# Kernel tuning notes

Measured on AMD Instinct MI355X. Metric: run time of the kernel, lower is better.

The kernel has to match this reference:

```python
import jax, jax.numpy as jnp
import numpy as np

N = 500_000
IN_CH = 64
OUT_CH = 32
HEADS = 4
NUM_SEGS = 1024


def setup_inputs() -> dict:
    key = jax.random.key(0)
    ks = jax.random.split(key, 8)
    x = jax.random.normal(ks[0], (N, IN_CH), dtype=jnp.float32)
    batch = jnp.sort(jax.random.randint(ks[1], (N,), 0, NUM_SEGS, dtype=jnp.int32))
    batch = batch.at[-1].set(NUM_SEGS - 1)  # mimic size = batch[-1]+1 == NUM_SEGS
    s_in = 1.0 / np.sqrt(IN_CH)
    s_hg = 1.0 / np.sqrt(HEADS * IN_CH)
    s_hm = 1.0 / np.sqrt(OUT_CH * HEADS)
    # gate_nn: Linear(in, heads*in, bias=False) -> PReLU -> Linear(heads*in, heads, bias=False)
    gate_w1 = jax.random.uniform(ks[2], (HEADS * IN_CH, IN_CH), jnp.float32, -s_in, s_in)
    prelu_a = jnp.asarray(0.25, dtype=jnp.float32)
    gate_w2 = jax.random.uniform(ks[3], (HEADS, HEADS * IN_CH), jnp.float32, -s_hg, s_hg)
    # nn: Linear(in, out*heads) -> ReLU -> Linear(out*heads, out*heads)
    mlp_w1 = jax.random.uniform(ks[4], (OUT_CH * HEADS, IN_CH), jnp.float32, -s_in, s_in)
    mlp_b1 = jax.random.uniform(ks[5], (OUT_CH * HEADS,), jnp.float32, -s_in, s_in)
    mlp_w2 = jax.random.uniform(ks[6], (OUT_CH * HEADS, OUT_CH * HEADS), jnp.float32, -s_hm, s_hm)
    mlp_b2 = jax.random.uniform(ks[7], (OUT_CH * HEADS,), jnp.float32, -s_hm, s_hm)
    return {"x": x, "batch": batch, "num_segments": NUM_SEGS,
            "gate_w1": gate_w1, "prelu_a": prelu_a, "gate_w2": gate_w2,
            "mlp_w1": mlp_w1, "mlp_b1": mlp_b1, "mlp_w2": mlp_w2, "mlp_b2": mlp_b2}


def reference(x, batch, num_segments, gate_w1, prelu_a, gate_w2,
              mlp_w1, mlp_b1, mlp_w2, mlp_b2):
    n = x.shape[0]
    # gate network: [N, heads]
    h = x @ gate_w1.T
    h = jnp.where(h >= 0, h, prelu_a * h)  # PReLU (shared scalar slope)
    gate = h @ gate_w2.T
    # feature MLP: [N, heads, out]
    feat = jax.nn.relu(x @ mlp_w1.T + mlp_b1) @ mlp_w2.T + mlp_b2
    feat = feat.reshape(n, HEADS, -1)
    # segment (per-graph) softmax over nodes, per head
    gmax = jax.ops.segment_max(gate, batch, num_segments=num_segments)  # [S, heads]
    escore = jnp.exp(gate - gmax[batch])
    denom = jax.ops.segment_sum(escore, batch, num_segments=num_segments)
    score = escore / (denom[batch] + 1e-16)  # [N, heads]
    # weighted scatter-add pooling
    out = jax.ops.segment_sum(score[..., None] * feat, batch, num_segments=num_segments)
    return out.reshape(num_segments, -1)  # [S, heads*out]
```

## Files before the change

kernel.cpp:

```cpp
#include <hip/hip_runtime.h>
#include <cstdint>
#include <cstddef>

#define NN 500000
#define NG 15625
#define NBLK 1536
#define NWAVES (NBLK * 2)

typedef __attribute__((ext_vector_type(8))) short short8;
typedef __attribute__((ext_vector_type(4))) float floatx4;
typedef __attribute__((ext_vector_type(4))) float fv4;

__device__ __forceinline__ unsigned short f2bf(float f) {
  union { float f; unsigned u; } v; v.f = f;
  unsigned r = v.u + 0x7FFFu + ((v.u >> 16) & 1u);
  return (unsigned short)(r >> 16);
}
__device__ __forceinline__ unsigned cvtpk(float a, float b) {
  unsigned r;
  asm("v_cvt_pk_bf16_f32 %0, %1, %2" : "=v"(r) : "v"(a), "v"(b));
  return r;
}
__device__ __forceinline__ fv4 ntload4(const float* p) {
  return __builtin_nontemporal_load((const fv4*)p);
}
__device__ __forceinline__ float bflo(unsigned u) {
  union { unsigned u; float f; } v; v.u = u << 16; return v.f;
}
__device__ __forceinline__ float bfhi(unsigned u) {
  union { unsigned u; float f; } v; v.u = u & 0xffff0000u; return v.f;
}

#define MFMA16(a, b, c) __builtin_amdgcn_mfma_f32_16x16x32_bf16((a), (b), (c), 0, 0, 0)

__global__ void swizzle_weights(const float* __restrict__ gw1, const float* __restrict__ mw1,
                                const float* __restrict__ gw2,
                                unsigned short* __restrict__ gw1s,
                                unsigned short* __restrict__ mw1s,
                                unsigned short* __restrict__ gw2s,
                                float* __restrict__ denom, float* __restrict__ zws) {
  int e = blockIdx.x * 256 + threadIdx.x;
  if (e < 4096) denom[e] = 0.f;
#pragma unroll
  for (int i = 0; i < 19; ++i) {
    int o = e + i * 28672;
    if (o < 524288) zws[o] = 0.f;
  }
  if (e >= 24576) {
    int local = e - 24576;
    int j = local & 7, lane = (local >> 3) & 63, s = local >> 9;
    int row = lane & 15, quad = (lane >> 4) & 3;
    int w = s * 32 + ((j >> 2) << 4) + 4 * quad + (j & 3);
    gw2s[local] = (row < 4) ? f2bf(gw2[row * 256 + w]) : (unsigned short)0;
    return;
  }
  const float* src; unsigned short* dst; int local;
  if (e < 16384) { src = gw1; dst = gw1s; local = e; }
  else           { src = mw1; dst = mw1s; local = e - 16384; }
  int j = local & 7, lane = (local >> 3) & 63, tile = local >> 9;
  int ks = tile & 1, mtile = tile >> 1;
  int row = mtile * 16 + (lane & 15);
  int k   = ks * 32 + ((lane >> 4) & 3) * 8 + j;
  dst[local] = f2bf(src[row * 64 + k]);
}

#define FLUSH() do {                                                          \
  if (quad == 0) {                                                            \
    _Pragma("unroll") for (int mt_ = 0; mt_ < 8; ++mt_)                       \
      _Pragma("unroll") for (int r_ = 0; r_ < 4; ++r_)                        \
        atomicAdd(&zws[((size_t)cur_seg * 4 + r_) * 128 + mt_ * 16 + lcol],   \
                  acc[mt_][r_]);                                              \
  }                                                                           \
  _Pragma("unroll") for (int mt_ = 0; mt_ < 8; ++mt_)                         \
    acc[mt_] = (floatx4){0.f, 0.f, 0.f, 0.f};                                 \
  { float v_ = es; v_ += __shfl_xor(v_, 16); v_ += __shfl_xor(v_, 32);        \
    if (lane < 4) atomicAdd(&denom[cur_seg * 4 + lane], v_); }                \
  es = 0.f;                                                                   \
} while (0)

__global__ __launch_bounds__(128, 2) void fused_kernel(
    const float* __restrict__ x, const int* __restrict__ batch,
    const unsigned short* __restrict__ gw1s, const unsigned short* __restrict__ mw1s,
    const unsigned short* __restrict__ gw2s, const float* __restrict__ prelu_a,
    const float* __restrict__ b1, float* __restrict__ denom,
    float* __restrict__ zws) {
  const int t = threadIdx.x;
  const int wave = t >> 6, lane = t & 63;
  const int quad = lane >> 4, lcol = lane & 15;

  const float slope = prelu_a[0];
  const int W = blockIdx.x * 2 + wave;
  const int g0 = (int)(((long long)W * NG) / NWAVES);
  const int g1 = (int)(((long long)(W + 1) * NG) / NWAVES);

  float b1v[8];
#pragma unroll
  for (int mt = 0; mt < 8; ++mt) b1v[mt] = b1[mt * 16 + lcol];

  floatx4 acc[8];
#pragma unroll
  for (int mt = 0; mt < 8; ++mt) acc[mt] = (floatx4){0.f, 0.f, 0.f, 0.f};
  float es = 0.f;
  int fs = g0 * 32; if (fs > NN - 1) fs = NN - 1;
  int cur_seg = batch[fs];

  for (int g = g0; g < g1; ++g) {
    const int base = g * 32;
    int sv[2];
    short8 bx[2][2];
#pragma unroll
    for (int nt = 0; nt < 2; ++nt) {
      int node = base + nt * 16 + lcol;
      sv[nt] = batch[node];
      const float* xp = x + (size_t)node * 64 + quad * 8;
      fv4 v0 = ntload4(xp), v1 = ntload4(xp + 4);
      fv4 v2 = ntload4(xp + 32), v3 = ntload4(xp + 36);
      union { short8 s; unsigned u[4]; } u0, u1;
      u0.u[0] = cvtpk(v0[0], v0[1]); u0.u[1] = cvtpk(v0[2], v0[3]);
      u0.u[2] = cvtpk(v1[0], v1[1]); u0.u[3] = cvtpk(v1[2], v1[3]);
      u1.u[0] = cvtpk(v2[0], v2[1]); u1.u[1] = cvtpk(v2[2], v2[3]);
      u1.u[2] = cvtpk(v3[0], v3[1]); u1.u[3] = cvtpk(v3[2], v3[3]);
      bx[nt][0] = u0.s; bx[nt][1] = u1.s;
    }

    floatx4 cg0 = {0.f, 0.f, 0.f, 0.f}, cg1 = {0.f, 0.f, 0.f, 0.f};
#pragma unroll
    for (int sst = 0; sst < 8; ++sst) {
      union GB { short8 s; unsigned u[4]; } gb0, gb1;
#pragma unroll
      for (int half = 0; half < 2; ++half) {
        const int mt = sst * 2 + half;
        short8 a0 = *(const short8*)(gw1s + ((size_t)(mt * 2 + 0) * 64 + lane) * 8);
        short8 a1 = *(const short8*)(gw1s + ((size_t)(mt * 2 + 1) * 64 + lane) * 8);
        floatx4 c0 = {0.f, 0.f, 0.f, 0.f};
        c0 = MFMA16(a0, bx[0][0], c0);
        c0 = MFMA16(a1, bx[0][1], c0);
        floatx4 c1 = {0.f, 0.f, 0.f, 0.f};
        c1 = MFMA16(a0, bx[1][0], c1);
        c1 = MFMA16(a1, bx[1][1], c1);
        gb0.u[half * 2 + 0] = cvtpk(fmaxf(c0[0], slope * c0[0]),
                                    fmaxf(c0[1], slope * c0[1]));
        gb0.u[half * 2 + 1] = cvtpk(fmaxf(c0[2], slope * c0[2]),
                                    fmaxf(c0[3], slope * c0[3]));
        gb1.u[half * 2 + 0] = cvtpk(fmaxf(c1[0], slope * c1[0]),
                                    fmaxf(c1[1], slope * c1[1]));
        gb1.u[half * 2 + 1] = cvtpk(fmaxf(c1[2], slope * c1[2]),
                                    fmaxf(c1[3], slope * c1[3]));
      }
      short8 ga = *(const short8*)(gw2s + ((size_t)sst * 64 + lane) * 8);
      cg0 = MFMA16(ga, gb0.s, cg0);
      cg1 = MFMA16(ga, gb1.s, cg1);
    }
    float e0a[4], e1a[4];
#pragma unroll
    for (int hh = 0; hh < 4; ++hh) {
      e0a[hh] = __expf(cg0[hh]);
      e1a[hh] = __expf(cg1[hh]);
    }

    float ev[8]; int svb[8];
#pragma unroll
    for (int j = 0; j < 4; ++j) {
      int src = 4 * quad + j;
      svb[j]     = __shfl(sv[0], src);
      svb[4 + j] = __shfl(sv[1], src);
      float t0 = __shfl(e0a[0], src), t1 = __shfl(e0a[1], src);
      float t2 = __shfl(e0a[2], src), t3 = __shfl(e0a[3], src);
      float c01 = (lcol & 1) ? t1 : t0, c23 = (lcol & 1) ? t3 : t2;
      ev[j] = (lcol & 2) ? c23 : c01;
      t0 = __shfl(e1a[0], src); t1 = __shfl(e1a[1], src);
      t2 = __shfl(e1a[2], src); t3 = __shfl(e1a[3], src);
      c01 = (lcol & 1) ? t1 : t0; c23 = (lcol & 1) ? t3 : t2;
      ev[4 + j] = (lcol & 2) ? c23 : c01;
    }

    union BH { short8 s; unsigned u[4]; } zb[8];
#pragma unroll
    for (int mt = 0; mt < 8; ++mt) {
      short8 w0 = *(const short8*)(mw1s + ((size_t)(mt * 2 + 0) * 64 + lane) * 8);
      short8 w1 = *(const short8*)(mw1s + ((size_t)(mt * 2 + 1) * 64 + lane) * 8);
      float bb = b1v[mt];
      floatx4 c0 = {0.f, 0.f, 0.f, 0.f};
      c0 = MFMA16(bx[0][0], w0, c0);
      c0 = MFMA16(bx[0][1], w1, c0);
      floatx4 c1 = {0.f, 0.f, 0.f, 0.f};
      c1 = MFMA16(bx[1][0], w0, c1);
      c1 = MFMA16(bx[1][1], w1, c1);
      zb[mt].u[0] = cvtpk(fmaxf(c0[0] + bb, 0.f), fmaxf(c0[1] + bb, 0.f));
      zb[mt].u[1] = cvtpk(fmaxf(c0[2] + bb, 0.f), fmaxf(c0[3] + bb, 0.f));
      zb[mt].u[2] = cvtpk(fmaxf(c1[0] + bb, 0.f), fmaxf(c1[1] + bb, 0.f));
      zb[mt].u[3] = cvtpk(fmaxf(c1[2] + bb, 0.f), fmaxf(c1[3] + bb, 0.f));
    }

    int p = 0;
    while (p < 32) {
      int selv = (p >> 4) ? sv[1] : sv[0];
      int s = __shfl(selv, p & 15);
      if (s != cur_seg) { FLUSH(); cur_seg = s; }
      int cnt = (int)__popcll(__ballot(sv[0] == s)) +
                (int)__popcll(__ballot(sv[1] == s));
      union { unsigned u[4]; short8 s8; } ea;
#pragma unroll
      for (int jj = 0; jj < 4; ++jj) {
        float e0 = (lcol < 4 && svb[2 * jj] == s) ? ev[2 * jj] : 0.f;
        float e1 = (lcol < 4 && svb[2 * jj + 1] == s) ? ev[2 * jj + 1] : 0.f;
        ea.u[jj] = cvtpk(e0, e1);
        es += bflo(ea.u[jj]) + bfhi(ea.u[jj]);
      }
#pragma unroll
      for (int mt = 0; mt < 8; ++mt)
        acc[mt] = MFMA16(ea.s8, zb[mt].s, acc[mt]);
      p += (cnt >> 2);
    }
  }
  FLUSH();
}

__global__ __launch_bounds__(128) void finalize_kernel(
    const float* __restrict__ zws, const float* __restrict__ denom,
    const float* __restrict__ mw2, const float* __restrict__ b2,
    float* __restrict__ out) {
  __shared__ float zL[512];
  const int seg = blockIdx.x, t = threadIdx.x;
#pragma unroll
  for (int i = 0; i < 4; ++i) zL[t + i * 128] = zws[(size_t)seg * 512 + t + i * 128];
  __syncthreads();
  const int fcol = t, h = t >> 5;
  float d = denom[seg * 4 + h];
  const fv4* mrow = (const fv4*)(mw2 + (size_t)fcol * 128);
  const fv4* zrow = (const fv4*)(zL + h * 128);
  float a0 = 0.f, a1 = 0.f, a2 = 0.f, a3 = 0.f;
#pragma unroll 8
  for (int k = 0; k < 32; ++k) {
    fv4 w = mrow[k], z = zrow[k];
    a0 = fmaf(w[0], z[0], a0); a1 = fmaf(w[1], z[1], a1);
    a2 = fmaf(w[2], z[2], a2); a3 = fmaf(w[3], z[3], a3);
  }
  float acc = (a0 + a1) + (a2 + a3);
  out[(size_t)seg * 128 + fcol] = (d > 0.f) ? (acc / d + b2[fcol]) : 0.f;
}

extern "C" void kernel_launch(void* const* d_in, const int* in_sizes, int n_in,
                              void* d_out, int out_size, void* d_ws, size_t ws_size,
                              hipStream_t stream) {
  const float* x     = (const float*)d_in[0];
  const int*   batch = (const int*)d_in[1];
  const float* gw1 = (const float*)d_in[3];
  const float* pa  = (const float*)d_in[4];
  const float* gw2 = (const float*)d_in[5];
  const float* mw1 = (const float*)d_in[6];
  const float* mb1 = (const float*)d_in[7];
  const float* mw2 = (const float*)d_in[8];
  const float* mb2 = (const float*)d_in[9];
  float* out = (float*)d_out;

  char* ws = (char*)d_ws;
  float* denom = (float*)ws;
  unsigned short* gw1s = (unsigned short*)(ws + 16384);
  unsigned short* mw1s = (unsigned short*)(ws + 49152);
  unsigned short* gw2s = (unsigned short*)(ws + 65536);
  float* zws = (float*)(ws + 73728);

  swizzle_weights<<<112, 256, 0, stream>>>(gw1, mw1, gw2, gw1s, mw1s, gw2s,
                                           denom, zws);

  fused_kernel<<<NBLK, 128, 0, stream>>>(x, batch, gw1s, mw1s, gw2s,
                                         pa, mb1, denom, zws);

  finalize_kernel<<<1024, 128, 0, stream>>>(zws, denom, mw2, mb2, out);
}
```

Before: 267.3 us.

## Stage swizzled bf16 weights in LDS per block and drop the preprocessing kernel

```diff
diff --git a/kernel.cpp b/kernel.cpp
--- a/kernel.cpp
+++ b/kernel.cpp
@@ -4,8 +4,8 @@
 
 #define NN 500000
 #define NG 15625
-#define NBLK 1536
-#define NWAVES (NBLK * 2)
+#define NBLK 512
+#define NWAVES (NBLK * 4)
 
 typedef __attribute__((ext_vector_type(8))) short short8;
 typedef __attribute__((ext_vector_type(4))) float floatx4;
@@ -21,9 +21,6 @@
   asm("v_cvt_pk_bf16_f32 %0, %1, %2" : "=v"(r) : "v"(a), "v"(b));
   return r;
 }
-__device__ __forceinline__ fv4 ntload4(const float* p) {
-  return __builtin_nontemporal_load((const fv4*)p);
-}
 __device__ __forceinline__ float bflo(unsigned u) {
   union { unsigned u; float f; } v; v.u = u << 16; return v.f;
 }
@@ -32,37 +29,6 @@
 }
 
 #define MFMA16(a, b, c) __builtin_amdgcn_mfma_f32_16x16x32_bf16((a), (b), (c), 0, 0, 0)
-
-__global__ void swizzle_weights(const float* __restrict__ gw1, const float* __restrict__ mw1,
-                                const float* __restrict__ gw2,
-                                unsigned short* __restrict__ gw1s,
-                                unsigned short* __restrict__ mw1s,
-                                unsigned short* __restrict__ gw2s,
-                                float* __restrict__ denom, float* __restrict__ zws) {
-  int e = blockIdx.x * 256 + threadIdx.x;
-  if (e < 4096) denom[e] = 0.f;
-#pragma unroll
-  for (int i = 0; i < 19; ++i) {
-    int o = e + i * 28672;
-    if (o < 524288) zws[o] = 0.f;
-  }
-  if (e >= 24576) {
-    int local = e - 24576;
-    int j = local & 7, lane = (local >> 3) & 63, s = local >> 9;
-    int row = lane & 15, quad = (lane >> 4) & 3;
-    int w = s * 32 + ((j >> 2) << 4) + 4 * quad + (j & 3);
-    gw2s[local] = (row < 4) ? f2bf(gw2[row * 256 + w]) : (unsigned short)0;
-    return;
-  }
-  const float* src; unsigned short* dst; int local;
-  if (e < 16384) { src = gw1; dst = gw1s; local = e; }
-  else           { src = mw1; dst = mw1s; local = e - 16384; }
-  int j = local & 7, lane = (local >> 3) & 63, tile = local >> 9;
-  int ks = tile & 1, mtile = tile >> 1;
-  int row = mtile * 16 + (lane & 15);
-  int k   = ks * 32 + ((lane >> 4) & 3) * 8 + j;
-  dst[local] = f2bf(src[row * 64 + k]);
-}
 
 #define FLUSH() do {                                                          \
   if (quad == 0) {                                                            \
@@ -78,18 +44,43 @@
   es = 0.f;                                                                   \
 } while (0)
 
-__global__ __launch_bounds__(128, 2) void fused_kernel(
+__global__ __launch_bounds__(256, 2) void fused_kernel(
     const float* __restrict__ x, const int* __restrict__ batch,
-    const unsigned short* __restrict__ gw1s, const unsigned short* __restrict__ mw1s,
-    const unsigned short* __restrict__ gw2s, const float* __restrict__ prelu_a,
+    const float* __restrict__ gw1, const float* __restrict__ mw1,
+    const float* __restrict__ gw2, const float* __restrict__ prelu_a,
     const float* __restrict__ b1, float* __restrict__ denom,
     float* __restrict__ zws) {
+  __shared__ unsigned short wl[28672];
   const int t = threadIdx.x;
+
+#pragma unroll 4
+  for (int e = t; e < 28672; e += 256) {
+    unsigned short v;
+    if (e < 24576) {
+      const float* src = (e < 16384) ? gw1 : mw1;
+      int local = (e < 16384) ? e : e - 16384;
+      int j = local & 7, lane = (local >> 3) & 63, tile = local >> 9;
+      int row = (tile >> 1) * 16 + (lane & 15);
+      int k = (tile & 1) * 32 + ((lane >> 4) & 3) * 8 + j;
+      v = f2bf(src[row * 64 + k]);
+    } else {
+      int local = e - 24576;
+      int j = local & 7, lane = (local >> 3) & 63, s = local >> 9;
+      int row = lane & 15, q = (lane >> 4) & 3;
+      int w = s * 32 + ((j >> 2) << 4) + 4 * q + (j & 3);
+      v = (row < 4) ? f2bf(gw2[row * 256 + w]) : (unsigned short)0;
+    }
+    wl[e] = v;
+  }
+  __syncthreads();
+  const unsigned short* gw1s = wl;
+  const unsigned short* mw1s = wl + 16384;
+  const unsigned short* gw2s = wl + 24576;
+
   const int wave = t >> 6, lane = t & 63;
   const int quad = lane >> 4, lcol = lane & 15;
-
   const float slope = prelu_a[0];
-  const int W = blockIdx.x * 2 + wave;
+  const int W = blockIdx.x * 4 + wave;
   const int g0 = (int)(((long long)W * NG) / NWAVES);
   const int g1 = (int)(((long long)(W + 1) * NG) / NWAVES);
 
@@ -113,8 +104,8 @@
       int node = base + nt * 16 + lcol;
       sv[nt] = batch[node];
       const float* xp = x + (size_t)node * 64 + quad * 8;
-      fv4 v0 = ntload4(xp), v1 = ntload4(xp + 4);
-      fv4 v2 = ntload4(xp + 32), v3 = ntload4(xp + 36);
+      fv4 v0 = *(const fv4*)xp,        v1 = *(const fv4*)(xp + 4);
+      fv4 v2 = *(const fv4*)(xp + 32), v3 = *(const fv4*)(xp + 36);
       union { short8 s; unsigned u[4]; } u0, u1;
       u0.u[0] = cvtpk(v0[0], v0[1]); u0.u[1] = cvtpk(v0[2], v0[3]);
       u0.u[2] = cvtpk(v1[0], v1[1]); u0.u[3] = cvtpk(v1[2], v1[3]);
@@ -256,15 +247,12 @@
 
   char* ws = (char*)d_ws;
   float* denom = (float*)ws;
-  unsigned short* gw1s = (unsigned short*)(ws + 16384);
-  unsigned short* mw1s = (unsigned short*)(ws + 49152);
-  unsigned short* gw2s = (unsigned short*)(ws + 65536);
-  float* zws = (float*)(ws + 73728);
-
-  swizzle_weights<<<112, 256, 0, stream>>>(gw1, mw1, gw2, gw1s, mw1s, gw2s,
-                                           denom, zws);
-
-  fused_kernel<<<NBLK, 128, 0, stream>>>(x, batch, gw1s, mw1s, gw2s,
+  float* zws   = (float*)(ws + 16384);
+
+  hipMemsetAsync(denom, 0, 16384, stream);
+  hipMemsetAsync(zws, 0, 2097152, stream);
+
+  fused_kernel<<<NBLK, 256, 0, stream>>>(x, batch, gw1, mw1, gw2,
                                          pa, mb1, denom, zws);
 
   finalize_kernel<<<1024, 128, 0, stream>>>(zws, denom, mw2, mb2, out);
```

Result: faster. 259.9 us (-2.7%).
